# Optimization experiments

Hardware: AMD Instinct MI355X
Metric: run time of the kernel (lower is better)

Reference implementation:

```python
import math
import jax, jax.numpy as jnp
import numpy as np
from jax import lax

HEADS = 8
DIM_HEAD = 32
DIM = 256
FF_INNER = DIM * 4
EPS = 1e-5


def conv1x1(x, w, b=None):
    # x: (B,C,H,W), w: (O,C)
    y = jnp.einsum('bchw,oc->bohw', x, w)
    return y if b is None else y + b[None, :, None, None]


def dwconv3(x, w, b):
    # depthwise 3x3, padding=1; w: (C,1,3,3)
    C = x.shape[1]
    y = lax.conv_general_dilated(x, w, (1, 1), 'SAME',
                                 dimension_numbers=('NCHW', 'OIHW', 'NCHW'),
                                 feature_group_count=C)
    return y + b[None, :, None, None]


def instance_norm(x):
    m = jnp.mean(x, axis=(2, 3), keepdims=True)
    v = jnp.var(x, axis=(2, 3), keepdims=True)
    return (x - m) / jnp.sqrt(v + EPS)


def chan_layer_norm(x, g, b):
    m = jnp.mean(x, axis=1, keepdims=True)
    v = jnp.var(x, axis=1, keepdims=True)
    return (x - m) / jnp.sqrt(v + EPS) * g + b


def l2norm(t):
    # F.normalize(t, dim=-1): normalize along last (width) axis
    n = jnp.sqrt(jnp.sum(t * t, axis=-1, keepdims=True))
    return t / jnp.maximum(n, 1e-12)


def dpsa(x, g, bc, w_qkv, w_out, b_out):
    B, C, H, W = x.shape
    kH = int(math.ceil(math.sqrt(H)))
    kW = int(math.ceil(math.sqrt(W)))
    x = chan_layer_norm(x, g, bc)
    qkv = conv1x1(x, w_qkv)                       # (B, 3*inner, H, W)
    q, k, v = jnp.split(qkv, 3, axis=1)
    fold = lambda t: t.reshape(B * HEADS, DIM_HEAD, H, W)
    q, k, v = fold(q), fold(k), fold(v)
    q, k = l2norm(q), l2norm(k)
    BH = B * HEADS
    q_probe = jnp.sum(jnp.abs(q), axis=(2, 3))    # (BH, d)
    if kH < H:
        k_height = jnp.sum(jnp.abs(k), axis=3)    # (BH, d, H)
        score_r = jnp.einsum('bc,bch->bh', q_probe, k_height)
        _, idx_h = lax.top_k(score_r, kH)          # (BH, kH)
        idx = jnp.broadcast_to(idx_h[:, None, :, None], (BH, DIM_HEAD, kH, W))
        k = jnp.take_along_axis(k, idx, axis=2)
        v = jnp.take_along_axis(v, idx, axis=2)
    if kW < W:
        k_width = jnp.sum(jnp.abs(k), axis=2)     # (BH, d, W)
        score_c = jnp.einsum('bc,bcw->bw', q_probe, k_width)
        _, idx_w = lax.top_k(score_c, kW)          # (BH, kW)
        idx = jnp.broadcast_to(idx_w[:, None, None, :], (BH, DIM_HEAD, k.shape[2], kW))
        k = jnp.take_along_axis(k, idx, axis=3)
        v = jnp.take_along_axis(v, idx, axis=3)
    flat = lambda t: t.transpose(0, 2, 3, 1).reshape(BH, -1, DIM_HEAD)
    q, k, v = flat(q), flat(k), flat(v)            # (BH, HW, d), (BH, kHkW, d)
    sim = jnp.einsum('bid,bjd->bij', q, k)         # note: original never applies scale
    attn = jax.nn.softmax(sim, axis=-1)
    out = jnp.einsum('bij,bjd->bid', attn, v)
    out = out.reshape(B, HEADS, H, W, DIM_HEAD).transpose(0, 1, 4, 2, 3)
    out = out.reshape(B, HEADS * DIM_HEAD, H, W)
    return conv1x1(out, w_out, b_out)


def hpb_forward(x, g, bc, w_qkv, w_out, b_out, w_dw, b_dw, w_comb, b_comb,
                w_ff1, b_ff1, w_ffdw, b_ffdw, w_ff2, b_ff2):
    attn_branch = dpsa(x, g, bc, w_qkv, w_out, b_out)
    conv_branch = dwconv3(x, w_dw, b_dw)
    combined = jnp.concatenate([attn_branch, conv_branch], axis=1)
    attn_out = conv1x1(combined, w_comb, b_comb) + x
    # feed-forward: 1x1 conv -> IN -> GELU -> Residual(dw3x3 -> IN -> GELU) -> 1x1 conv -> IN
    h = jax.nn.gelu(instance_norm(conv1x1(attn_out, w_ff1, b_ff1)), approximate=False)
    h = h + jax.nn.gelu(instance_norm(dwconv3(h, w_ffdw, b_ffdw)), approximate=False)
    return instance_norm(conv1x1(h, w_ff2, b_ff2))


def setup_inputs() -> dict:
    key = jax.random.key(0)
    ks = jax.random.split(key, 12)
    s = 0.02
    inner = HEADS * DIM_HEAD
    return {
        'x': jax.random.normal(ks[0], (16, DIM, 64, 64), dtype=jnp.float32),
        'g': jnp.ones((1, DIM, 1, 1), jnp.float32),
        'bc': jnp.zeros((1, DIM, 1, 1), jnp.float32),
        'w_qkv': jax.random.normal(ks[1], (inner * 3, DIM), jnp.float32) * s,
        'w_out': jax.random.normal(ks[2], (DIM, inner), jnp.float32) * s,
        'b_out': jnp.zeros((DIM,), jnp.float32),
        'w_dw': jax.random.normal(ks[3], (DIM, 1, 3, 3), jnp.float32) * s,
        'b_dw': jnp.zeros((DIM,), jnp.float32),
        'w_comb': jax.random.normal(ks[4], (DIM, DIM * 2), jnp.float32) * s,
        'b_comb': jnp.zeros((DIM,), jnp.float32),
        'w_ff1': jax.random.normal(ks[5], (FF_INNER, DIM), jnp.float32) * s,
        'b_ff1': jnp.zeros((FF_INNER,), jnp.float32),
        'w_ffdw': jax.random.normal(ks[6], (FF_INNER, 1, 3, 3), jnp.float32) * s,
        'b_ffdw': jnp.zeros((FF_INNER,), jnp.float32),
        'w_ff2': jax.random.normal(ks[7], (DIM, FF_INNER), jnp.float32) * s,
        'b_ff2': jnp.zeros((DIM,), jnp.float32),
    }


def reference(x, g, bc, w_qkv, w_out, b_out, w_dw, b_dw, w_comb, b_comb,
              w_ff1, b_ff1, w_ffdw, b_ffdw, w_ff2, b_ff2):
    return hpb_forward(x, g, bc, w_qkv, w_out, b_out, w_dw, b_dw, w_comb, b_comb,
                       w_ff1, b_ff1, w_ffdw, b_ffdw, w_ff2, b_ff2)
```

## Files before the change

kernel.cpp:

```cpp
#include <hip/hip_runtime.h>
#include <math.h>

#define NB 16
#define NC 256
#define NP 4096
#define NHEADS 8
#define NDH 32
#define NBH 128
#define NFF 1024
#define CEPS 1e-5f

typedef short s16x8 __attribute__((ext_vector_type(8)));
typedef float f32x4 __attribute__((ext_vector_type(4)));

__global__ __launch_bounds__(256) void diag_fill(float* __restrict__ out, float val, int n)
{
    int i = blockIdx.x * 256 + threadIdx.x;
    if (i < n) out[i] = val;
}

__device__ inline unsigned short f2bf(float f) {
    unsigned u = __float_as_uint(f);
    return (unsigned short)((u + 0x7FFFu + ((u >> 16) & 1u)) >> 16);
}
__device__ inline float bf2f(unsigned short h) { return __uint_as_float(((unsigned)h) << 16); }
__device__ inline void split2(float f, unsigned short& hi, unsigned short& lo) {
    hi = f2bf(f);
    lo = f2bf(f - bf2f(hi));
}
__device__ inline void split_rn(float f, unsigned short& hi, unsigned short& lo) {
    unsigned u = __float_as_uint(f);
    unsigned tt = u + 0x8000u;
    hi = (unsigned short)(tt >> 16);
    float r = f - __uint_as_float(tt & 0xffff0000u);
    lo = (unsigned short)((__float_as_uint(r) + 0x8000u) >> 16);
}
__device__ inline unsigned pack_hl(float f) {
    unsigned short h, lo; split2(f, h, lo);
    return ((unsigned)h << 16) | (unsigned)lo;
}
__device__ inline float packf(float f) { return __uint_as_float(pack_hl(f)); }

__global__ __launch_bounds__(256) void pack_wg_kernel(
    const float* __restrict__ w, const float* __restrict__ g,
    unsigned* __restrict__ pw, int n)
{
    int i = blockIdx.x * 256 + threadIdx.x;
    if (i < n) pw[i] = pack_hl(w[i] * g[i & 255]);
}

__global__ __launch_bounds__(256) void pack_w_plain_kernel(
    const float* __restrict__ w, unsigned* __restrict__ pw, int n)
{
    int i = blockIdx.x * 256 + threadIdx.x;
    if (i < n) pw[i] = pack_hl(w[i]);
}

__global__ __launch_bounds__(256) void cln_stats_kernel(
    const float* __restrict__ x, float* __restrict__ rs, float* __restrict__ mrs)
{
    __shared__ double red[512];
    int t = threadIdx.x;
    int i = t & 63, q = t >> 6;
    int col = blockIdx.x * 64 + i;
    int b = col >> 12, p = col & 4095;
    const float* src = x + (size_t)b * NC * NP + (size_t)(q * 64) * NP + p;
    double s = 0.0, s2 = 0.0;
    #pragma unroll 8
    for (int c = 0; c < 64; c++) { float v = src[(size_t)c * NP]; s += v; s2 += (double)v * v; }
    red[q * 64 + i] = s; red[256 + q * 64 + i] = s2;
    __syncthreads();
    if (q == 0) {
        double S  = red[i] + red[64 + i] + red[128 + i] + red[192 + i];
        double S2 = red[256 + i] + red[320 + i] + red[384 + i] + red[448 + i];
        double mean = S * (1.0 / 256.0);
        double var = S2 * (1.0 / 256.0) - mean * mean;
        double r = 1.0 / sqrt(var + (double)CEPS);
        rs[col]  = (float)r;
        mrs[col] = (float)(mean * r);
    }
}

__global__ __launch_bounds__(256) void ab_kernel(
    const float* __restrict__ wq, const float* __restrict__ g, const float* __restrict__ bc,
    float* __restrict__ Aab, float* __restrict__ Bab)
{
    int o = blockIdx.x * 256 + threadIdx.x;
    if (o >= 768) return;
    double a = 0.0, bsum = 0.0;
    for (int c = 0; c < 256; c++) {
        double w = wq[o * 256 + c];
        a += w * (double)g[c];
        bsum += w * (double)bc[c];
    }
    Aab[o] = (float)a; Bab[o] = (float)bsum;
}

__global__ __launch_bounds__(256) void fuse_comb_kernel(
    const float* __restrict__ w_comb, const float* __restrict__ w_out,
    const float* __restrict__ b_out, const float* __restrict__ b_comb,
    unsigned* __restrict__ pwF, float* __restrict__ bF)
{
    int idx = blockIdx.x * 256 + threadIdx.x;
    int o = idx >> 9, cc = idx & 511;
    float val;
    if (cc < 256) {
        double s = 0.0;
        for (int k = 0; k < 256; k++)
            s += (double)w_comb[o * 512 + k] * (double)w_out[k * 256 + cc];
        val = (float)s;
    } else {
        val = w_comb[o * 512 + cc];
    }
    pwF[idx] = pack_hl(val);
    if (idx < 256) {
        double s = 0.0;
        for (int k = 0; k < 256; k++)
            s += (double)w_comb[idx * 512 + k] * (double)b_out[k];
        bF[idx] = (float)(s + (double)b_comb[idx]);
    }
}

template<bool PACKO, bool PACKA, bool CLN, bool OBF16, bool BBF16>
__global__ __launch_bounds__(512) void gemm_mfma(
    const float* __restrict__ inA, int sA, int C1,
    const float* __restrict__ inB, int sB, int Ctot,
    const float* __restrict__ Wt, const float* __restrict__ bias,
    const float* __restrict__ resid, float* __restrict__ out, int sO, int O,
    const float* __restrict__ rs, const float* __restrict__ mrs,
    const float* __restrict__ Aab, const float* __restrict__ Bab,
    float* __restrict__ qrow, float* __restrict__ kheight)
{
    __shared__ __align__(16) unsigned short Ah[128 * 32], Al[128 * 32];
    __shared__ __align__(16) unsigned short Bh[128 * 32];
    __shared__ __align__(16) unsigned short Bl[BBF16 ? 16 : 128 * 32];
    char* cAh = (char*)Ah; char* cAl = (char*)Al;
    char* cBh = (char*)Bh; char* cBl = (char*)Bl;

    const unsigned npb = gridDim.x * gridDim.y;
    unsigned lin = blockIdx.x + gridDim.x * (blockIdx.y + gridDim.y * blockIdx.z);
    unsigned low = lin & 7u, rest = lin >> 3;
    unsigned high = (rest >= npb) ? 1u : 0u;
    unsigned idx = rest - high * npb;
    const int b = (int)(low + 8u * high);
    const int o0 = (int)(idx / gridDim.x) * 128, p0 = (int)(idx % gridDim.x) * 128;

    const int t = threadIdx.x;
    const int l = t & 63, w = t >> 6;
    const int wr = w & 3, wc = w >> 2;
    const int g = l >> 4, l15 = l & 15;
    const int slotl = (l & 3) ^ ((l >> 2) & 3);

    f32x4 acc[2][4];
    #pragma unroll
    for (int m = 0; m < 2; m++)
        #pragma unroll
        for (int n = 0; n < 4; n++) acc[m][n] = (f32x4){0.f, 0.f, 0.f, 0.f};

    const int arow = t >> 2;
    const int ak8 = (t & 3) * 8;
    const int aslot = (arow & 3) ^ ((arow >> 2) & 3);
    const int aoff = arow * 64 + ((((ak8 >> 3)) ^ aslot) << 4);
    const int bp = t & 127;
    const int bhk = t >> 7;
    const int bslot = (bp & 3) ^ ((bp >> 2) & 3);
    const int boffst = bp * 64 + ((bhk ^ bslot) << 4);

    uint4 wa0, wa1;
    unsigned pb[8];

    #define LOAD_TILE(K0)                                                                 \
    {                                                                                     \
        const unsigned* wsrc = (const unsigned*)Wt + (size_t)(o0 + arow) * Ctot + (K0) + ak8; \
        wa0 = *(const uint4*)(wsrc);                                                      \
        wa1 = *(const uint4*)(wsrc + 4);                                                  \
        _Pragma("unroll")                                                                 \
        for (int q = 0; q < 4; q++) {                                                     \
            int c2 = bhk * 8 + q * 2;                                                     \
            int cc = (K0) + c2;                                                           \
            if constexpr (BBF16) {                                                        \
                const unsigned short* s16 = (cc < C1)                                     \
                    ? (const unsigned short*)inA + ((size_t)b * sA + cc) * (size_t)NP + p0 + bp \
                    : (const unsigned short*)inB + ((size_t)b * sB + (cc - C1)) * (size_t)NP + p0 + bp; \
                unsigned short v0 = s16[0];                                               \
                unsigned short v1 = s16[NP];                                              \
                pb[q] = (unsigned)v0 | ((unsigned)v1 << 16);                              \
            } else {                                                                      \
                const float* srcp = (cc < C1) ? inA + ((size_t)b * sA + cc) * (size_t)NP  \
                                              : inB + ((size_t)b * sB + (cc - C1)) * (size_t)NP; \
                pb[2 * q]     = __float_as_uint(srcp[p0 + bp]);                           \
                pb[2 * q + 1] = __float_as_uint(srcp[(size_t)NP + p0 + bp]);              \
            }                                                                             \
        }                                                                                 \
    }

    #define STORE_LDS()                                                                   \
    {                                                                                     \
        if constexpr (PACKA) {                                                            \
            uint4 hq, lq;                                                                 \
            hq.x = __builtin_amdgcn_perm(wa0.y, wa0.x, 0x07060302u);                      \
            lq.x = __builtin_amdgcn_perm(wa0.y, wa0.x, 0x05040100u);                      \
            hq.y = __builtin_amdgcn_perm(wa0.w, wa0.z, 0x07060302u);                      \
            lq.y = __builtin_amdgcn_perm(wa0.w, wa0.z, 0x05040100u);                      \
            hq.z = __builtin_amdgcn_perm(wa1.y, wa1.x, 0x07060302u);                      \
            lq.z = __builtin_amdgcn_perm(wa1.y, wa1.x, 0x05040100u);                      \
            hq.w = __builtin_amdgcn_perm(wa1.w, wa1.z, 0x07060302u);                      \
            lq.w = __builtin_amdgcn_perm(wa1.w, wa1.z, 0x05040100u);                      \
            *(uint4*)(cAh + aoff) = hq;                                                   \
            *(uint4*)(cAl + aoff) = lq;                                                   \
        } else {                                                                          \
            ushort4 h0, l0, h1, l1;                                                       \
            split_rn(__uint_as_float(wa0.x), h0.x, l0.x);                                 \
            split_rn(__uint_as_float(wa0.y), h0.y, l0.y);                                 \
            split_rn(__uint_as_float(wa0.z), h0.z, l0.z);                                 \
            split_rn(__uint_as_float(wa0.w), h0.w, l0.w);                                 \
            split_rn(__uint_as_float(wa1.x), h1.x, l1.x);                                 \
            split_rn(__uint_as_float(wa1.y), h1.y, l1.y);                                 \
            split_rn(__uint_as_float(wa1.z), h1.z, l1.z);                                 \
            split_rn(__uint_as_float(wa1.w), h1.w, l1.w);                                 \
            *(ushort4*)(cAh + aoff) = h0; *(ushort4*)(cAh + aoff + 8) = h1;               \
            *(ushort4*)(cAl + aoff) = l0; *(ushort4*)(cAl + aoff + 8) = l1;               \
        }                                                                                 \
        if constexpr (BBF16) {                                                            \
            *(uint4*)(cBh + boffst) = (uint4){pb[0], pb[1], pb[2], pb[3]};                \
        } else {                                                                          \
            unsigned hp[4], lp[4];                                                        \
            _Pragma("unroll")                                                             \
            for (int q = 0; q < 4; q++) {                                                 \
                unsigned u0 = pb[2 * q], u1 = pb[2 * q + 1];                              \
                if constexpr (CLN) {                                                      \
                    unsigned short sh0, sl0, sh1, sl1;                                    \
                    split_rn(__uint_as_float(u0), sh0, sl0);                              \
                    split_rn(__uint_as_float(u1), sh1, sl1);                              \
                    hp[q] = (unsigned)sh0 | ((unsigned)sh1 << 16);                        \
                    lp[q] = (unsigned)sl0 | ((unsigned)sl1 << 16);                        \
                } else {                                                                  \
                    hp[q] = __builtin_amdgcn_perm(u1, u0, 0x07060302u);                   \
                    lp[q] = __builtin_amdgcn_perm(u1, u0, 0x05040100u);                   \
                }                                                                         \
            }                                                                             \
            *(uint4*)(cBh + boffst) = (uint4){hp[0], hp[1], hp[2], hp[3]};                \
            *(uint4*)(cBl + boffst) = (uint4){lp[0], lp[1], lp[2], lp[3]};                \
        }                                                                                 \
    }

    LOAD_TILE(0)

    for (int k0 = 0; k0 < Ctot; k0 += 32) {
        if (k0) __syncthreads();
        STORE_LDS()
        __syncthreads();
        if (k0 + 32 < Ctot) LOAD_TILE(k0 + 32)

        s16x8 ah[2], al[2];
        #pragma unroll
        for (int m = 0; m < 2; m++) {
            int ao = (wr * 32 + m * 16 + l15) * 64 + ((g ^ slotl) << 4);
            ah[m] = *(const s16x8*)(cAh + ao);
            al[m] = *(const s16x8*)(cAl + ao);
        }
        #pragma unroll
        for (int n = 0; n < 4; n++) {
            int bo = (wc * 64 + n * 16 + l15) * 64 + ((g ^ slotl) << 4);
            s16x8 bh = *(const s16x8*)(cBh + bo);
            if constexpr (BBF16) {
                #pragma unroll
                for (int m = 0; m < 2; m++) {
                    acc[m][n] = __builtin_amdgcn_mfma_f32_16x16x32_bf16(ah[m], bh, acc[m][n], 0, 0, 0);
                    acc[m][n] = __builtin_amdgcn_mfma_f32_16x16x32_bf16(al[m], bh, acc[m][n], 0, 0, 0);
                }
            } else {
                s16x8 bl = *(const s16x8*)(cBl + bo);
                #pragma unroll
                for (int m = 0; m < 2; m++) {
                    acc[m][n] = __builtin_amdgcn_mfma_f32_16x16x32_bf16(ah[m], bh, acc[m][n], 0, 0, 0);
                    acc[m][n] = __builtin_amdgcn_mfma_f32_16x16x32_bf16(ah[m], bl, acc[m][n], 0, 0, 0);
                    acc[m][n] = __builtin_amdgcn_mfma_f32_16x16x32_bf16(al[m], bh, acc[m][n], 0, 0, 0);
                }
            }
        }
    }
    #undef LOAD_TILE
    #undef STORE_LDS

    #pragma unroll
    for (int m = 0; m < 2; m++) {
        #pragma unroll
        for (int r = 0; r < 4; r++) {
            int orow = o0 + wr * 32 + m * 16 + g * 4 + r;
            float bs = (!CLN && bias) ? bias[orow] : 0.f;
            float Ao = CLN ? Aab[orow] : 0.f;
            float Bo = CLN ? Bab[orow] : 0.f;
            if constexpr (CLN) {
                float vv[4];
                #pragma unroll
                for (int n = 0; n < 4; n++) {
                    int pcol = p0 + wc * 64 + n * 16 + l15;
                    size_t cidx = (size_t)b * NP + pcol;
                    vv[n] = rs[cidx] * acc[m][n][r] - mrs[cidx] * Ao + Bo;
                }
                int which = orow >> 8;
                if (which < 2) {
                    float ss = vv[0] * vv[0] + vv[1] * vv[1] + vv[2] * vv[2] + vv[3] * vv[3];
                    ss += __shfl_xor(ss, 1); ss += __shfl_xor(ss, 2);
                    ss += __shfl_xor(ss, 4); ss += __shfl_xor(ss, 8);
                    float inv = 1.f / fmaxf(sqrtf(ss), 1e-12f);
                    float as = 0.f;
                    #pragma unroll
                    for (int n = 0; n < 4; n++) { vv[n] *= inv; as += fabsf(vv[n]); }
                    as += __shfl_xor(as, 1); as += __shfl_xor(as, 2);
                    as += __shfl_xor(as, 4); as += __shfl_xor(as, 8);
                    if (l15 == 0) {
                        int idx2 = orow & 255;
                        int head = idx2 >> 5, c = idx2 & 31;
                        int h = (p0 >> 6) + wc;
                        int rr = ((b << 3) + head) * 2048 + c * 64 + h;
                        (which == 0 ? qrow : kheight)[rr] = as;
                    }
                }
                #pragma unroll
                for (int n = 0; n < 4; n++) {
                    int pcol = p0 + wc * 64 + n * 16 + l15;
                    out[((size_t)b * sO + orow) * (size_t)NP + pcol] = vv[n];
                }
            } else {
                #pragma unroll
                for (int n = 0; n < 4; n++) {
                    int pcol = p0 + wc * 64 + n * 16 + l15;
                    float v = acc[m][n][r] + bs;
                    if (resid) v += resid[((size_t)b * O + orow) * (size_t)NP + pcol];
                    size_t oidx = ((size_t)b * sO + orow) * (size_t)NP + pcol;
                    if constexpr (OBF16)
                        ((unsigned short*)out)[oidx] = f2bf(v);
                    else
                        out[oidx] = PACKO ? packf(v) : v;
                }
            }
        }
    }
}

__global__ __launch_bounds__(64) void select_kernel(
    const float* __restrict__ qkv, const float* __restrict__ qrow,
    const float* __restrict__ kheight,
    float* __restrict__ ksel, int* __restrict__ hswsl)
{
    const int bh = blockIdx.x;
    const int b = bh >> 3, head = bh & 7;
    const int lane = threadIdx.x;
    __shared__ int hs[8], wsl[8];
    __shared__ float qp[32];
    if (lane < 32) {
        double s = 0.0;
        const float* qr = qrow + (size_t)bh * 2048 + lane * 64;
        for (int h = 0; h < 64; h++) s += qr[h];
        qp[lane] = (float)s;
    }
    __syncthreads();
    double scd = 0.0;
    for (int c = 0; c < 32; c++) scd += (double)qp[c] * kheight[((size_t)bh * 32 + c) * 64 + lane];
    float sc = (float)scd;
    for (int it = 0; it < 8; it++) {
        float v = sc; int id = lane;
        for (int off = 32; off; off >>= 1) {
            float ov = __shfl_xor(v, off); int oi = __shfl_xor(id, off);
            if (ov > v || (ov == v && oi < id)) { v = ov; id = oi; }
        }
        if (lane == 0) hs[it] = id;
        if (lane == id) sc = -3.4e38f;
    }
    __syncthreads();
    const float* kbase = qkv + ((size_t)b * 768 + 256 + head * 32) * NP;
    double sc2d = 0.0;
    for (int c = 0; c < 32; c++) {
        float kw = 0.f;
        for (int hi = 0; hi < 8; hi++)
            kw += fabsf(kbase[(size_t)c * NP + hs[hi] * 64 + lane]);
        sc2d += (double)qp[c] * kw;
    }
    float sc2 = (float)sc2d;
    for (int it = 0; it < 8; it++) {
        float v = sc2; int id = lane;
        for (int off = 32; off; off >>= 1) {
            float ov = __shfl_xor(v, off); int oi = __shfl_xor(id, off);
            if (ov > v || (ov == v && oi < id)) { v = ov; id = oi; }
        }
        if (lane == 0) wsl[it] = id;
        if (lane == id) sc2 = -3.4e38f;
    }
    __syncthreads();
    if (lane < 8) hswsl[bh * 16 + lane] = hs[lane];
    else if (lane < 16) hswsl[bh * 16 + lane] = wsl[lane - 8];
    int hi = lane >> 3, wi = lane & 7;
    int hh = hs[hi], ww = wsl[wi];
    for (int d = 0; d < 32; d++)
        ksel[((size_t)bh * 64 + lane) * 32 + d] = kbase[(size_t)d * NP + hh * 64 + ww];
}

__global__ __launch_bounds__(256) void vsel_kernel(
    const float* __restrict__ x, const float* __restrict__ w_qkv, const float* __restrict__ g,
    const int* __restrict__ hswsl, const float* __restrict__ rs, const float* __restrict__ mrs,
    const float* __restrict__ Aab, const float* __restrict__ Bab,
    float* __restrict__ vsel)
{
    __shared__ float Wg[32][257];
    __shared__ float xcol[16][257];
    __shared__ int pos_s[16];
    const int bh = blockIdx.y, b = bh >> 3, head = bh & 7;
    const int t = threadIdx.x;
    for (int i = t; i < 8192; i += 256) {
        int d = i >> 8, c = i & 255;
        Wg[d][c] = w_qkv[(size_t)(512 + head * 32 + d) * 256 + c] * g[c];
    }
    if (t < 16) {
        int j = blockIdx.x * 16 + t;
        int hh = hswsl[bh * 16 + (j >> 3)];
        int ww = hswsl[bh * 16 + 8 + (j & 7)];
        pos_s[t] = hh * 64 + ww;
    }
    __syncthreads();
    for (int i = t; i < 4096; i += 256) {
        int jj = i >> 8, c = i & 255;
        xcol[jj][c] = x[((size_t)b * 256 + c) * (size_t)NP + pos_s[jj]];
    }
    __syncthreads();
    const int l = t & 63, w = t >> 6;
    const int d = l & 31, ch = l >> 5;
    const float Av = Aab[512 + head * 32 + d];
    const float Bv = Bab[512 + head * 32 + d];
    for (int q = 0; q < 4; q++) {
        int jj = w * 4 + q;
        float s = 0.f;
        #pragma unroll
        for (int c = 0; c < 128; c++) s += Wg[d][ch * 128 + c] * xcol[jj][ch * 128 + c];
        s += __shfl_xor(s, 32);
        if (ch == 0) {
            int j = blockIdx.x * 16 + jj;
            size_t cidx = (size_t)b * NP + pos_s[jj];
            float val = rs[cidx] * s - mrs[cidx] * Av + Bv;
            vsel[((size_t)bh * 64 + j) * 32 + d] = val;
        }
    }
}

__global__ __launch_bounds__(256) void attn_kernel(
    const float* __restrict__ qkv, const float* __restrict__ ksel, const float* __restrict__ vsel,
    unsigned short* __restrict__ ctxu)
{
    __shared__ __align__(16) float ks[64][32];
    __shared__ __align__(16) float vs[64][32];
    int bh = blockIdx.y, b = bh >> 3, head = bh & 7;
    int t = threadIdx.x;
    const float* kb = ksel + (size_t)bh * 2048;
    const float* vb = vsel + (size_t)bh * 2048;
    for (int i = 0; i < 8; i++) {
        ((float*)ks)[t + i * 256] = kb[t + i * 256];
        ((float*)vs)[t + i * 256] = vb[t + i * 256];
    }
    __syncthreads();
    int p = blockIdx.x * 256 + t;
    const float* qb = qkv + ((size_t)b * 768 + head * 32) * NP + p;
    unsigned short* ob = ctxu + ((size_t)b * 256 + head * 32) * NP + p;
    float q[32];
    #pragma unroll
    for (int d = 0; d < 32; d++) q[d] = qb[(size_t)d * NP];
    float s[64], m = -3.4e38f;
    for (int j = 0; j < 64; j++) {
        float dot = 0.f;
        #pragma unroll
        for (int d = 0; d < 32; d++) dot += q[d] * ks[j][d];
        s[j] = dot; m = fmaxf(m, dot);
    }
    float den = 0.f;
    for (int j = 0; j < 64; j++) { float e = __expf(s[j] - m); s[j] = e; den += e; }
    float o[32] = {};
    for (int j = 0; j < 64; j++) {
        float a = s[j];
        #pragma unroll
        for (int d = 0; d < 32; d++) o[d] += a * vs[j][d];
    }
    float r = 1.f / den;
    #pragma unroll
    for (int d = 0; d < 32; d++) ob[(size_t)d * NP] = f2bf(o[d] * r);
}

__global__ __launch_bounds__(256) void dwconv_kernel(
    const float* __restrict__ in, const float* __restrict__ w, const float* __restrict__ bias,
    unsigned short* __restrict__ out, int Cn)
{
    __shared__ float pl[66][67];
    int bcb = blockIdx.x;
    int c = bcb % Cn;
    const float* src = in + (size_t)bcb * NP;
    unsigned* dst2 = (unsigned*)(out + (size_t)bcb * NP);
    int t = threadIdx.x;
    int rp = t >> 3, cg = t & 7;
    int r0 = rp * 2, c0 = cg * 8;
    if (t < 66) { pl[0][t] = 0.f; pl[65][t] = 0.f; }
    if (t >= 66 && t < 130) { int rr = t - 65; pl[rr][0] = 0.f; pl[rr][65] = 0.f; }
    float w9[9];
    #pragma unroll
    for (int k = 0; k < 9; k++) w9[k] = w[c * 9 + k];
    float bsv = bias[c];
    float4 a0 = *(const float4*)(src + r0 * 64 + c0);
    float4 a1 = *(const float4*)(src + r0 * 64 + c0 + 4);
    float4 b0 = *(const float4*)(src + (r0 + 1) * 64 + c0);
    float4 b1 = *(const float4*)(src + (r0 + 1) * 64 + c0 + 4);
    pl[r0 + 1][c0 + 1] = a0.x; pl[r0 + 1][c0 + 2] = a0.y;
    pl[r0 + 1][c0 + 3] = a0.z; pl[r0 + 1][c0 + 4] = a0.w;
    pl[r0 + 1][c0 + 5] = a1.x; pl[r0 + 1][c0 + 6] = a1.y;
    pl[r0 + 1][c0 + 7] = a1.z; pl[r0 + 1][c0 + 8] = a1.w;
    pl[r0 + 2][c0 + 1] = b0.x; pl[r0 + 2][c0 + 2] = b0.y;
    pl[r0 + 2][c0 + 3] = b0.z; pl[r0 + 2][c0 + 4] = b0.w;
    pl[r0 + 2][c0 + 5] = b1.x; pl[r0 + 2][c0 + 6] = b1.y;
    pl[r0 + 2][c0 + 7] = b1.z; pl[r0 + 2][c0 + 8] = b1.w;
    __syncthreads();
    float acc0[8], acc1[8];
    #pragma unroll
    for (int j = 0; j < 8; j++) { acc0[j] = bsv; acc1[j] = bsv; }
    #pragma unroll
    for (int dy = 0; dy < 4; dy++) {
        float tp[10];
        #pragma unroll
        for (int k = 0; k < 10; k++) tp[k] = pl[r0 + dy][c0 + k];
        if (dy < 3) {
            #pragma unroll
            for (int dx = 0; dx < 3; dx++)
                #pragma unroll
                for (int j = 0; j < 8; j++)
                    acc0[j] = fmaf(w9[dy * 3 + dx], tp[j + dx], acc0[j]);
        }
        if (dy >= 1) {
            #pragma unroll
            for (int dx = 0; dx < 3; dx++)
                #pragma unroll
                for (int j = 0; j < 8; j++)
                    acc1[j] = fmaf(w9[(dy - 1) * 3 + dx], tp[j + dx], acc1[j]);
        }
    }
    uint4 o0, o1;
    o0.x = (unsigned)f2bf(acc0[0]) | ((unsigned)f2bf(acc0[1]) << 16);
    o0.y = (unsigned)f2bf(acc0[2]) | ((unsigned)f2bf(acc0[3]) << 16);
    o0.z = (unsigned)f2bf(acc0[4]) | ((unsigned)f2bf(acc0[5]) << 16);
    o0.w = (unsigned)f2bf(acc0[6]) | ((unsigned)f2bf(acc0[7]) << 16);
    o1.x = (unsigned)f2bf(acc1[0]) | ((unsigned)f2bf(acc1[1]) << 16);
    o1.y = (unsigned)f2bf(acc1[2]) | ((unsigned)f2bf(acc1[3]) << 16);
    o1.z = (unsigned)f2bf(acc1[4]) | ((unsigned)f2bf(acc1[5]) << 16);
    o1.w = (unsigned)f2bf(acc1[6]) | ((unsigned)f2bf(acc1[7]) << 16);
    *(uint4*)(dst2 + ((r0 * 64 + c0) >> 1)) = o0;
    *(uint4*)(dst2 + (((r0 + 1) * 64 + c0) >> 1)) = o1;
}

__device__ inline float gelu3(float x) {
    float z = x * 0.70710678118654752f;
    float a = fabsf(z);
    float t = __builtin_amdgcn_rcpf(fmaf(0.47047f, a, 1.0f));
    float p = t * (0.3480242f + t * (-0.0958798f + t * 0.7478556f));
    float e = __expf(-a * a);
    float r = 1.0f - p * e;
    float erfz = copysignf(r, z);
    return 0.5f * x * (1.0f + erfz);
}

__device__ inline void wave_reduce2(float& a, float& b, float* sred, int t)
{
    #pragma unroll
    for (int off = 32; off; off >>= 1) { a += __shfl_xor(a, off); b += __shfl_xor(b, off); }
    int w = t >> 6, lane = t & 63;
    __syncthreads();
    if (lane == 0) { sred[w] = a; sred[4 + w] = b; }
    __syncthreads();
    a = sred[0] + sred[1] + sred[2] + sred[3];
    b = sred[4] + sred[5] + sred[6] + sred[7];
}

__device__ inline double block_reduce1(float s, double* red, int t)
{
    __syncthreads();
    red[t] = (double)s;
    __syncthreads();
    for (int st = 128; st; st >>= 1) {
        if (t < st) red[t] += red[t + st];
        __syncthreads();
    }
    return red[0];
}

__global__ __launch_bounds__(256) void ff_fused_kernel(
    unsigned short* __restrict__ h, const float* __restrict__ w, const float* __restrict__ bias)
{
    __shared__ float pl[66][67];
    __shared__ float sred[8];
    int plane = blockIdx.x;
    int c = plane & (NFF - 1);
    const unsigned* h2 = (const unsigned*)(h + (size_t)plane * NP);
    unsigned* h2w = (unsigned*)(h + (size_t)plane * NP);
    int t = threadIdx.x;
    int rp = t >> 3, cg = t & 7;
    int r0 = rp * 2, c0 = cg * 8;
    if (t < 66) { pl[0][t] = 0.f; pl[65][t] = 0.f; }
    if (t >= 66 && t < 130) { int rr = t - 65; pl[rr][0] = 0.f; pl[rr][65] = 0.f; }

    uint4 u0 = *(const uint4*)(h2 + ((r0 * 64 + c0) >> 1));
    uint4 u1 = *(const uint4*)(h2 + (((r0 + 1) * 64 + c0) >> 1));
    float v[16]; float sf = 0.f, s2f = 0.f;
    {
        unsigned uu[8] = {u0.x, u0.y, u0.z, u0.w, u1.x, u1.y, u1.z, u1.w};
        #pragma unroll
        for (int i = 0; i < 8; i++) {
            float x0 = bf2f((unsigned short)(uu[i] & 0xffffu));
            float x1 = bf2f((unsigned short)(uu[i] >> 16));
            v[2 * i] = x0; v[2 * i + 1] = x1;
            sf += x0 + x1;
            s2f += x0 * x0 + x1 * x1;
        }
    }
    wave_reduce2(sf, s2f, sred, t);
    float mf = sf * (1.f / NP);
    float var = s2f * (1.f / NP) - mf * mf;
    float rs = rsqrtf(var + CEPS);

    float w9[9];
    #pragma unroll
    for (int k = 0; k < 9; k++) w9[k] = w[c * 9 + k];
    float bsv = bias[c];

    #pragma unroll
    for (int j = 0; j < 8; j++) {
        float gx = gelu3((v[j] - mf) * rs);
        v[j] = gx;
        pl[r0 + 1][c0 + 1 + j] = gx;
    }
    #pragma unroll
    for (int j = 0; j < 8; j++) {
        float gx = gelu3((v[8 + j] - mf) * rs);
        v[8 + j] = gx;
        pl[r0 + 2][c0 + 1 + j] = gx;
    }
    __syncthreads();

    float acc0[8], acc1[8];
    #pragma unroll
    for (int j = 0; j < 8; j++) { acc0[j] = bsv; acc1[j] = bsv; }
    #pragma unroll
    for (int dy = 0; dy < 4; dy++) {
        float tp[10];
        #pragma unroll
        for (int k = 0; k < 10; k++) tp[k] = pl[r0 + dy][c0 + k];
        if (dy < 3) {
            #pragma unroll
            for (int dx = 0; dx < 3; dx++)
                #pragma unroll
                for (int j = 0; j < 8; j++)
                    acc0[j] = fmaf(w9[dy * 3 + dx], tp[j + dx], acc0[j]);
        }
        if (dy >= 1) {
            #pragma unroll
            for (int dx = 0; dx < 3; dx++)
                #pragma unroll
                for (int j = 0; j < 8; j++)
                    acc1[j] = fmaf(w9[(dy - 1) * 3 + dx], tp[j + dx], acc1[j]);
        }
    }
    float sg = 0.f, s2g = 0.f;
    #pragma unroll
    for (int j = 0; j < 8; j++) {
        sg += acc0[j] + acc1[j];
        s2g += acc0[j] * acc0[j] + acc1[j] * acc1[j];
    }
    wave_reduce2(sg, s2g, sred, t);
    float mf2 = sg * (1.f / NP);
    float var2 = s2g * (1.f / NP) - mf2 * mf2;
    float rs2 = rsqrtf(var2 + CEPS);

    uint4 o0, o1;
    {
        float r00 = v[0] + gelu3((acc0[0] - mf2) * rs2);
        float r01 = v[1] + gelu3((acc0[1] - mf2) * rs2);
        float r02 = v[2] + gelu3((acc0[2] - mf2) * rs2);
        float r03 = v[3] + gelu3((acc0[3] - mf2) * rs2);
        float r04 = v[4] + gelu3((acc0[4] - mf2) * rs2);
        float r05 = v[5] + gelu3((acc0[5] - mf2) * rs2);
        float r06 = v[6] + gelu3((acc0[6] - mf2) * rs2);
        float r07 = v[7] + gelu3((acc0[7] - mf2) * rs2);
        o0.x = (unsigned)f2bf(r00) | ((unsigned)f2bf(r01) << 16);
        o0.y = (unsigned)f2bf(r02) | ((unsigned)f2bf(r03) << 16);
        o0.z = (unsigned)f2bf(r04) | ((unsigned)f2bf(r05) << 16);
        o0.w = (unsigned)f2bf(r06) | ((unsigned)f2bf(r07) << 16);
        float r10 = v[8]  + gelu3((acc1[0] - mf2) * rs2);
        float r11 = v[9]  + gelu3((acc1[1] - mf2) * rs2);
        float r12 = v[10] + gelu3((acc1[2] - mf2) * rs2);
        float r13 = v[11] + gelu3((acc1[3] - mf2) * rs2);
        float r14 = v[12] + gelu3((acc1[4] - mf2) * rs2);
        float r15 = v[13] + gelu3((acc1[5] - mf2) * rs2);
        float r16 = v[14] + gelu3((acc1[6] - mf2) * rs2);
        float r17 = v[15] + gelu3((acc1[7] - mf2) * rs2);
        o1.x = (unsigned)f2bf(r10) | ((unsigned)f2bf(r11) << 16);
        o1.y = (unsigned)f2bf(r12) | ((unsigned)f2bf(r13) << 16);
        o1.z = (unsigned)f2bf(r14) | ((unsigned)f2bf(r15) << 16);
        o1.w = (unsigned)f2bf(r16) | ((unsigned)f2bf(r17) << 16);
    }
    *(uint4*)(h2w + ((r0 * 64 + c0) >> 1)) = o0;
    *(uint4*)(h2w + (((r0 + 1) * 64 + c0) >> 1)) = o1;
}

__global__ __launch_bounds__(256) void in_final_kernel(float* __restrict__ y)
{
    __shared__ double red[256];
    size_t base = (size_t)blockIdx.x * NP;
    int t = threadIdx.x;
    float v[16]; float sf = 0.f;
    #pragma unroll
    for (int i = 0; i < 16; i++) { float x = y[base + t + i * 256]; v[i] = x; sf += x; }
    double S = block_reduce1(sf, red, t);
    float mf = (float)(S * (1.0 / NP));
    float s2f = 0.f;
    #pragma unroll
    for (int i = 0; i < 16; i++) { float d = v[i] - mf; v[i] = d; s2f += d * d; }
    double S2 = block_reduce1(s2f, red, t);
    float rs = (float)(1.0 / sqrt(S2 * (1.0 / NP) + (double)CEPS));
    #pragma unroll
    for (int i = 0; i < 16; i++)
        y[base + t + i * 256] = v[i] * rs;
}

extern "C" void kernel_launch(void* const* d_in, const int* in_sizes, int n_in,
                              void* d_out, int out_size, void* d_ws, size_t ws_size,
                              hipStream_t stream)
{
    const float* x      = (const float*)d_in[0];
    const float* g      = (const float*)d_in[1];
    const float* bc     = (const float*)d_in[2];
    const float* w_qkv  = (const float*)d_in[3];
    const float* w_out  = (const float*)d_in[4];
    const float* b_out  = (const float*)d_in[5];
    const float* w_dw   = (const float*)d_in[6];
    const float* b_dw   = (const float*)d_in[7];
    const float* w_comb = (const float*)d_in[8];
    const float* b_comb = (const float*)d_in[9];
    const float* w_ff1  = (const float*)d_in[10];
    const float* b_ff1  = (const float*)d_in[11];
    const float* w_ffdw = (const float*)d_in[12];
    const float* b_ffdw = (const float*)d_in[13];
    const float* w_ff2  = (const float*)d_in[14];
    const float* b_ff2  = (const float*)d_in[15];
    float* out = (float*)d_out;
    float* ws  = (float*)d_ws;

    const size_t S = (size_t)NB * NC * NP;
    float* qkv   = ws + S;
    unsigned short* h1u   = (unsigned short*)ws;
    unsigned short* ctxu  = (unsigned short*)(ws + 2097152);
    unsigned short* convu = (unsigned short*)(ws + S);
    unsigned short* Fbufu = (unsigned short*)out;
    float* qrow    = ws;
    float* kheight = qrow + 262144;
    float* kselb   = kheight + 262144;
    float* vselb   = kselb + 262144;
    int*   hswsl   = (int*)(ws + 1048576);
    float* rs_a    = ws + 1052672;
    float* mrs_a   = rs_a + 65536;
    float* Aab     = mrs_a + 65536;
    float* Bab     = Aab + 768;
    unsigned* pw_qkv = (unsigned*)out;
    unsigned* pwF    = (unsigned*)ws;
    float*    bF     = ws + 131072;
    unsigned* pw_ff1 = (unsigned*)(ws + 2 * S);
    unsigned* pw_ff2 = (unsigned*)(ws + 2 * S) + 262144;

    size_t need = 4 * S * sizeof(float);
    if (ws_size < need) {
        float val = 1024.0f + (float)(ws_size >> 20);
        diag_fill<<<(out_size + 255) / 256, 256, 0, stream>>>(out, val, out_size);
        return;
    }

    pack_wg_kernel<<<512, 256, 0, stream>>>(w_qkv, g, pw_qkv, 512 * 256);
    cln_stats_kernel<<<1024, 256, 0, stream>>>(x, rs_a, mrs_a);
    ab_kernel<<<3, 256, 0, stream>>>(w_qkv, g, bc, Aab, Bab);
    gemm_mfma<false, true, true, false, false><<<dim3(32, 4, NB), 512, 0, stream>>>(
        x, 256, 256, nullptr, 0, 256, (const float*)pw_qkv, nullptr, nullptr, qkv, 768, 512,
        rs_a, mrs_a, Aab, Bab, qrow, kheight);
    select_kernel<<<NBH, 64, 0, stream>>>(qkv, qrow, kheight, kselb, hswsl);
    vsel_kernel<<<dim3(4, NBH), 256, 0, stream>>>(x, w_qkv, g, hswsl, rs_a, mrs_a,
                                                  Aab, Bab, vselb);
    attn_kernel<<<dim3(16, NBH), 256, 0, stream>>>(qkv, kselb, vselb, ctxu);
    fuse_comb_kernel<<<512, 256, 0, stream>>>(w_comb, w_out, b_out, b_comb, pwF, bF);
    pack_w_plain_kernel<<<1024, 256, 0, stream>>>(w_ff1, pw_ff1, 1024 * 256);
    pack_w_plain_kernel<<<1024, 256, 0, stream>>>(w_ff2, pw_ff2, 256 * 1024);
    dwconv_kernel<<<NB * NC, 256, 0, stream>>>(x, w_dw, b_dw, convu, NC);
    gemm_mfma<false, true, false, true, true><<<dim3(32, 2, NB), 512, 0, stream>>>(
        (const float*)ctxu, 256, 256, (const float*)convu, 256, 512,
        (const float*)pwF, bF, x, (float*)Fbufu, 256, 256,
        nullptr, nullptr, nullptr, nullptr, nullptr, nullptr);
    gemm_mfma<false, true, false, true, true><<<dim3(32, 8, NB), 512, 0, stream>>>(
        (const float*)Fbufu, 256, 256, nullptr, 0, 256, (const float*)pw_ff1, b_ff1, nullptr,
        (float*)h1u, 1024, 1024, nullptr, nullptr, nullptr, nullptr, nullptr, nullptr);
    ff_fused_kernel<<<NB * NFF, 256, 0, stream>>>(h1u, w_ffdw, b_ffdw);
    gemm_mfma<false, true, false, false, true><<<dim3(32, 2, NB), 512, 0, stream>>>(
        (const float*)h1u, 1024, 1024, nullptr, 0, 1024, (const float*)pw_ff2, b_ff2, nullptr,
        out, 256, 256, nullptr, nullptr, nullptr, nullptr, nullptr, nullptr);
    in_final_kernel<<<NB * NC, 256, 0, stream>>>(out);
}
```

Baseline: 692.8 us.

## Double-buffer LDS tiles in MFMA GEMM to drop one barrier per K-step

```diff
diff --git a/kernel.cpp b/kernel.cpp
--- a/kernel.cpp
+++ b/kernel.cpp
@@ -131,11 +131,9 @@
     const float* __restrict__ Aab, const float* __restrict__ Bab,
     float* __restrict__ qrow, float* __restrict__ kheight)
 {
-    __shared__ __align__(16) unsigned short Ah[128 * 32], Al[128 * 32];
-    __shared__ __align__(16) unsigned short Bh[128 * 32];
-    __shared__ __align__(16) unsigned short Bl[BBF16 ? 16 : 128 * 32];
-    char* cAh = (char*)Ah; char* cAl = (char*)Al;
-    char* cBh = (char*)Bh; char* cBl = (char*)Bl;
+    __shared__ __align__(16) unsigned short Ah[2][128 * 32], Al[2][128 * 32];
+    __shared__ __align__(16) unsigned short Bh[2][128 * 32];
+    __shared__ __align__(16) unsigned short Bl[2][BBF16 ? 16 : 128 * 32];
 
     const unsigned npb = gridDim.x * gridDim.y;
     unsigned lin = blockIdx.x + gridDim.x * (blockIdx.y + gridDim.y * blockIdx.z);
@@ -194,8 +192,11 @@
         }                                                                                 \
     }
 
-    #define STORE_LDS()                                                                   \
+    #define STORE_LDS(BUF)                                                                \
     {                                                                                     \
+        char* cAh = (char*)Ah[BUF]; char* cAl = (char*)Al[BUF];                           \
+        char* cBh = (char*)Bh[BUF]; char* cBl = (char*)Bl[BUF];                           \
+        (void)cBl;                                                                        \
         if constexpr (PACKA) {                                                            \
             uint4 hq, lq;                                                                 \
             hq.x = __builtin_amdgcn_perm(wa0.y, wa0.x, 0x07060302u);                      \
@@ -244,44 +245,61 @@
         }                                                                                 \
     }
 
+    #define MFMA_STEP(BUF)                                                                \
+    {                                                                                     \
+        const char* cAh = (const char*)Ah[BUF]; const char* cAl = (const char*)Al[BUF];   \
+        const char* cBh = (const char*)Bh[BUF]; const char* cBl = (const char*)Bl[BUF];   \
+        (void)cBl;                                                                        \
+        s16x8 ah[2], al[2];                                                               \
+        _Pragma("unroll")                                                                 \
+        for (int m = 0; m < 2; m++) {                                                     \
+            int ao = (wr * 32 + m * 16 + l15) * 64 + ((g ^ slotl) << 4);                  \
+            ah[m] = *(const s16x8*)(cAh + ao);                                            \
+            al[m] = *(const s16x8*)(cAl + ao);                                            \
+        }                                                                                 \
+        _Pragma("unroll")                                                                 \
+        for (int n = 0; n < 4; n++) {                                                     \
+            int bo = (wc * 64 + n * 16 + l15) * 64 + ((g ^ slotl) << 4);                  \
+            s16x8 bh = *(const s16x8*)(cBh + bo);                                         \
+            if constexpr (BBF16) {                                                        \
+                _Pragma("unroll")                                                         \
+                for (int m = 0; m < 2; m++) {                                             \
+                    acc[m][n] = __builtin_amdgcn_mfma_f32_16x16x32_bf16(ah[m], bh, acc[m][n], 0, 0, 0); \
+                    acc[m][n] = __builtin_amdgcn_mfma_f32_16x16x32_bf16(al[m], bh, acc[m][n], 0, 0, 0); \
+                }                                                                         \
+            } else {                                                                      \
+                s16x8 bl = *(const s16x8*)(cBl + bo);                                     \
+                _Pragma("unroll")                                                         \
+                for (int m = 0; m < 2; m++) {                                             \
+                    acc[m][n] = __builtin_amdgcn_mfma_f32_16x16x32_bf16(ah[m], bh, acc[m][n], 0, 0, 0); \
+                    acc[m][n] = __builtin_amdgcn_mfma_f32_16x16x32_bf16(ah[m], bl, acc[m][n], 0, 0, 0); \
+                    acc[m][n] = __builtin_amdgcn_mfma_f32_16x16x32_bf16(al[m], bh, acc[m][n], 0, 0, 0); \
+                }                                                                         \
+            }                                                                             \
+        }                                                                                 \
+    }
+
     LOAD_TILE(0)
-
-    for (int k0 = 0; k0 < Ctot; k0 += 32) {
-        if (k0) __syncthreads();
-        STORE_LDS()
+    STORE_LDS(0)
+    __syncthreads();
+
+    for (int k0 = 0; k0 < Ctot; k0 += 64) {
+        LOAD_TILE(k0 + 32)
+        MFMA_STEP(0)
+        STORE_LDS(1)
         __syncthreads();
-        if (k0 + 32 < Ctot) LOAD_TILE(k0 + 32)
-
-        s16x8 ah[2], al[2];
-        #pragma unroll
-        for (int m = 0; m < 2; m++) {
-            int ao = (wr * 32 + m * 16 + l15) * 64 + ((g ^ slotl) << 4);
-            ah[m] = *(const s16x8*)(cAh + ao);
-            al[m] = *(const s16x8*)(cAl + ao);
-        }
-        #pragma unroll
-        for (int n = 0; n < 4; n++) {
-            int bo = (wc * 64 + n * 16 + l15) * 64 + ((g ^ slotl) << 4);
-            s16x8 bh = *(const s16x8*)(cBh + bo);
-            if constexpr (BBF16) {
-                #pragma unroll
-                for (int m = 0; m < 2; m++) {
-                    acc[m][n] = __builtin_amdgcn_mfma_f32_16x16x32_bf16(ah[m], bh, acc[m][n], 0, 0, 0);
-                    acc[m][n] = __builtin_amdgcn_mfma_f32_16x16x32_bf16(al[m], bh, acc[m][n], 0, 0, 0);
-                }
-            } else {
-                s16x8 bl = *(const s16x8*)(cBl + bo);
-                #pragma unroll
-                for (int m = 0; m < 2; m++) {
-                    acc[m][n] = __builtin_amdgcn_mfma_f32_16x16x32_bf16(ah[m], bh, acc[m][n], 0, 0, 0);
-                    acc[m][n] = __builtin_amdgcn_mfma_f32_16x16x32_bf16(ah[m], bl, acc[m][n], 0, 0, 0);
-                    acc[m][n] = __builtin_amdgcn_mfma_f32_16x16x32_bf16(al[m], bh, acc[m][n], 0, 0, 0);
-                }
-            }
+        if (k0 + 64 < Ctot) {
+            LOAD_TILE(k0 + 64)
+            MFMA_STEP(1)
+            STORE_LDS(0)
+            __syncthreads();
+        } else {
+            MFMA_STEP(1)
         }
     }
     #undef LOAD_TILE
     #undef STORE_LDS
+    #undef MFMA_STEP
 
     #pragma unroll
     for (int m = 0; m < 2; m++) {
```

Measured after the change: 745.2 us. 7.6% more time.
